# Kernel optimization log

Hardware: AMD Instinct MI355X
Metric: run time of the kernel (lower is better)

Reference implementation:

```python
import jax, jax.numpy as jnp
import numpy as np

B, G, FI, FO, H, W = 16, 8, 64, 64, 64, 64
N_ITER = 3


def setup_inputs() -> dict:
    key = jax.random.key(0)
    kx, kw, kb = jax.random.split(key, 3)
    x = jax.random.normal(kx, (B, G * FI, H, W), dtype=jnp.float32)
    # kaiming_normal_ on [fo*g, fi, 1, 1]: std = sqrt(2 / fan_in), fan_in = fi*1*1
    weight = jax.random.normal(kw, (FO * G, FI, 1, 1), dtype=jnp.float32) * np.sqrt(2.0 / FI)
    bias = jax.random.normal(kb, (1, FO, 1, 1), dtype=jnp.float32) * 0.01
    return {"x": x, "weight": weight, "bias": bias}


def reference(x, weight, bias):
    g, n_iter = G, N_ITER
    gfo, fi = weight.shape[:2]
    fo = gfo // g
    b, c, h, w = x.shape
    # grouped 1x1 conv == per-group channel matmul
    xg = x.reshape(b, g, fi, h, w)
    wg = weight.reshape(g, fo, fi)
    con = jnp.einsum('bgihw,gfi->bgfhw', xg, wg)  # [B, g, fo, H, W]
    beta = jnp.zeros((), dtype=x.dtype)
    for i in range(n_iter):
        alpha = jax.nn.sigmoid(beta)
        v = jnp.sum(alpha * con, axis=1, keepdims=True)  # [B, 1, fo, H, W]
        if i == n_iter - 1:
            out = v[:, 0]  # [B, fo, H, W]
            return out + bias
        beta = beta + jnp.sum(v * con, axis=2, keepdims=True)  # [B, g, 1, H, W]
```

## Files before the change

### kernel.cpp

```cpp
#include <hip/hip_runtime.h>


typedef __attribute__((ext_vector_type(8))) _Float16 half8;
typedef __attribute__((ext_vector_type(4))) float f32x4;

#define NG   8
#define NFI  64
#define NFO  64
#define HW   4096

__device__ __forceinline__ float sigmoidf_fast(float v) {
    float e = __builtin_amdgcn_exp2f(-1.44269504088896f * v);
    return __builtin_amdgcn_rcpf(1.0f + e);
}

__global__ __launch_bounds__(256)
void wconv_kernel(const float* __restrict__ w, _Float16* __restrict__ wbuf) {
    int V = blockIdx.x * 256 + threadIdx.x;
    int g    = V >> 10;
    int t    = (V >> 8) & 3;
    int c    = (V >> 6) & 3;
    int lane = V & 63;
    int pl = lane & 15, q = lane >> 4;
    const float* src = w + g * (NFO * NFI) + (t * 16 + pl) * NFI + (c & 1) * 32 + q * 8;
    half8 o;
    #pragma unroll
    for (int j = 0; j < 8; ++j) {
        float f = src[j];
        _Float16 h = (_Float16)f;
        o[j] = (c >> 1) ? (_Float16)(f - (float)h) : h;
    }
    *(half8*)(wbuf + (size_t)V * 8) = o;
}

__global__ __launch_bounds__(256, 2)
void routing_kernel(const float* __restrict__ x,
                    const _Float16* __restrict__ wbuf,
                    const float* __restrict__ bias,
                    float* __restrict__ out) {
    const int tid  = threadIdx.x;
    const int b    = blockIdx.x >> 6;
    const int p0   = (blockIdx.x & 63) << 6;
    const int lane = tid & 63;
    const int wv   = tid >> 6;
    const int pl   = lane & 15;
    const int q    = lane >> 4;
    const int pw   = wv * 16 + pl;

    __shared__ float    xlds[2][64 * 64];
    __shared__ _Float16 wlds[2][16 * 512];

    const float* xbase = x + (size_t)b * (NG * NFI) * HW;

#define MKXS(c) \
    const int   ch##c = wv * 16 + (c) * 4 + q; \
    const float* xs##c = xbase + (size_t)ch##c * HW + p0 + ((pl * 4 - 8 * (ch##c >> 3)) & 63);
    MKXS(0) MKXS(1) MKXS(2) MKXS(3)
#undef MKXS

    const int rb0 = q * 512 + ((pw + 8 * q) & 63);
    const int rb1 = 2048 + q * 512 + ((pw + 8 * q + 32) & 63);

    f32x4 acc[NG][4];
    #pragma unroll
    for (int g = 0; g < NG; ++g)
        #pragma unroll
        for (int t = 0; t < 4; ++t)
            acc[g][t] = (f32x4){0.f, 0.f, 0.f, 0.f};

#define CB   asm volatile("" ::: "memory")
#define BAR  __builtin_amdgcn_s_barrier()
#define SB0  __builtin_amdgcn_sched_barrier(0)
#define WAITV(N) asm volatile("s_waitcnt vmcnt(" #N ")" ::: "memory")

#define WSTAGE(G, BUF)                                                        \
    {                                                                         \
        const _Float16* ws_ = wbuf + (size_t)(G) * 8192 + (wv * 4) * 512 + lane * 8; \
        _Float16* wd_ = &wlds[BUF][0] + (wv * 4) * 512;                       \
        __builtin_amdgcn_global_load_lds(                                     \
            (const __attribute__((address_space(1))) void*)(ws_),             \
            (__attribute__((address_space(3))) void*)(wd_), 16, 0, 0);        \
        __builtin_amdgcn_global_load_lds(                                     \
            (const __attribute__((address_space(1))) void*)(ws_ + 512),       \
            (__attribute__((address_space(3))) void*)(wd_ + 512), 16, 0, 0);  \
        __builtin_amdgcn_global_load_lds(                                     \
            (const __attribute__((address_space(1))) void*)(ws_ + 1024),      \
            (__attribute__((address_space(3))) void*)(wd_ + 1024), 16, 0, 0); \
        __builtin_amdgcn_global_load_lds(                                     \
            (const __attribute__((address_space(1))) void*)(ws_ + 1536),      \
            (__attribute__((address_space(3))) void*)(wd_ + 1536), 16, 0, 0); \
    }

#define XSTAGE(G, BUF)                                                        \
    {                                                                         \
        const size_t go_ = (size_t)(G) * 64 * HW;                             \
        float* xd_ = &xlds[BUF][0] + (wv * 16) * 64;                          \
        __builtin_amdgcn_global_load_lds(                                     \
            (const __attribute__((address_space(1))) void*)(xs0 + go_),       \
            (__attribute__((address_space(3))) void*)(xd_), 16, 0, 0);        \
        __builtin_amdgcn_global_load_lds(                                     \
            (const __attribute__((address_space(1))) void*)(xs1 + go_),       \
            (__attribute__((address_space(3))) void*)(xd_ + 256), 16, 0, 0);  \
        __builtin_amdgcn_global_load_lds(                                     \
            (const __attribute__((address_space(1))) void*)(xs2 + go_),       \
            (__attribute__((address_space(3))) void*)(xd_ + 512), 16, 0, 0);  \
        __builtin_amdgcn_global_load_lds(                                     \
            (const __attribute__((address_space(1))) void*)(xs3 + go_),       \
            (__attribute__((address_space(3))) void*)(xd_ + 768), 16, 0, 0);  \
    }

#define XGRP(G, BUF)                                                         \
    {                                                                        \
        const float* xr0_ = &xlds[BUF][0] + rb0;                             \
        const float* xr1_ = &xlds[BUF][0] + rb1;                             \
        half8 b0, b1;                                                        \
        b0[0] = (_Float16)xr0_[0 * 64]; b0[1] = (_Float16)xr0_[1 * 64];      \
        b0[2] = (_Float16)xr0_[2 * 64]; b0[3] = (_Float16)xr0_[3 * 64];      \
        b0[4] = (_Float16)xr0_[4 * 64]; b0[5] = (_Float16)xr0_[5 * 64];      \
        b0[6] = (_Float16)xr0_[6 * 64]; b0[7] = (_Float16)xr0_[7 * 64];      \
        b1[0] = (_Float16)xr1_[0 * 64]; b1[1] = (_Float16)xr1_[1 * 64];      \
        b1[2] = (_Float16)xr1_[2 * 64]; b1[3] = (_Float16)xr1_[3 * 64];      \
        b1[4] = (_Float16)xr1_[4 * 64]; b1[5] = (_Float16)xr1_[5 * 64];      \
        b1[6] = (_Float16)xr1_[6 * 64]; b1[7] = (_Float16)xr1_[7 * 64];      \
        const _Float16* wg_ = &wlds[BUF][0] + lane * 8;                      \
        _Pragma("unroll")                                                    \
        for (int t = 0; t < 4; ++t) {                                        \
            const _Float16* wp_ = wg_ + (size_t)t * 2048;                    \
            half8 a0h = *(const half8*)(wp_);                                \
            half8 a1h = *(const half8*)(wp_ + 512);                          \
            half8 a0l = *(const half8*)(wp_ + 1024);                         \
            half8 a1l = *(const half8*)(wp_ + 1536);                         \
            acc[G][t] = __builtin_amdgcn_mfma_f32_16x16x32_f16(a0h, b0, acc[G][t], 0, 0, 0); \
            acc[G][t] = __builtin_amdgcn_mfma_f32_16x16x32_f16(a1h, b1, acc[G][t], 0, 0, 0); \
            acc[G][t] = __builtin_amdgcn_mfma_f32_16x16x32_f16(a0l, b0, acc[G][t], 0, 0, 0); \
            acc[G][t] = __builtin_amdgcn_mfma_f32_16x16x32_f16(a1l, b1, acc[G][t], 0, 0, 0); \
        }                                                                    \
    }

    WSTAGE(0, 0); XSTAGE(0, 0); CB;
    WSTAGE(1, 1); XSTAGE(1, 1); CB;

    WAITV(8); BAR; SB0; XGRP(0, 0); BAR; WSTAGE(2, 0); XSTAGE(2, 0); CB;
    WAITV(8); BAR; SB0; XGRP(1, 1); BAR; WSTAGE(3, 1); XSTAGE(3, 1); CB;
    WAITV(8); BAR; SB0; XGRP(2, 0); BAR; WSTAGE(4, 0); XSTAGE(4, 0); CB;
    WAITV(8); BAR; SB0; XGRP(3, 1); BAR; WSTAGE(5, 1); XSTAGE(5, 1); CB;
    WAITV(8); BAR; SB0; XGRP(4, 0); BAR; WSTAGE(6, 0); XSTAGE(6, 0); CB;
    WAITV(8); BAR; SB0; XGRP(5, 1); BAR; WSTAGE(7, 1); XSTAGE(7, 1); CB;
    WAITV(8); BAR; SB0; XGRP(6, 0); BAR;
    WAITV(0); BAR; SB0; XGRP(7, 1);

#undef XGRP
#undef XSTAGE
#undef WSTAGE
#undef CB
#undef BAR
#undef SB0
#undef WAITV

    float v0[4][4];
    #pragma unroll
    for (int t = 0; t < 4; ++t)
        #pragma unroll
        for (int r = 0; r < 4; ++r) {
            float s = 0.f;
            #pragma unroll
            for (int g = 0; g < NG; ++g) s += acc[g][t][r];
            v0[t][r] = 0.5f * s;
        }

    float beta[NG], alpha[NG];
    #pragma unroll
    for (int g = 0; g < NG; ++g) {
        float s = 0.f;
        #pragma unroll
        for (int t = 0; t < 4; ++t)
            #pragma unroll
            for (int r = 0; r < 4; ++r)
                s += v0[t][r] * acc[g][t][r];
        s += __shfl_xor(s, 16);
        s += __shfl_xor(s, 32);
        beta[g]  = s;
        alpha[g] = sigmoidf_fast(s);
    }

    #pragma unroll
    for (int t = 0; t < 4; ++t)
        #pragma unroll
        for (int r = 0; r < 4; ++r) {
            float s = 0.f;
            #pragma unroll
            for (int g = 0; g < NG; ++g) s += alpha[g] * acc[g][t][r];
            v0[t][r] = s;
        }
    #pragma unroll
    for (int g = 0; g < NG; ++g) {
        float s = 0.f;
        #pragma unroll
        for (int t = 0; t < 4; ++t)
            #pragma unroll
            for (int r = 0; r < 4; ++r)
                s += v0[t][r] * acc[g][t][r];
        s += __shfl_xor(s, 16);
        s += __shfl_xor(s, 32);
        beta[g] += s;
        alpha[g] = sigmoidf_fast(beta[g]);
    }

    #pragma unroll
    for (int t = 0; t < 4; ++t)
        #pragma unroll
        for (int r = 0; r < 4; ++r) {
            int f = t * 16 + q * 4 + r;
            float s = bias[f];
            #pragma unroll
            for (int g = 0; g < NG; ++g) s += alpha[g] * acc[g][t][r];
            out[((size_t)(b * NFO + f)) * HW + p0 + pw] = s;
        }
}

extern "C" void kernel_launch(void* const* d_in, const int* in_sizes, int n_in,
                              void* d_out, int out_size, void* d_ws, size_t ws_size,
                              hipStream_t stream) {
    const float* x    = (const float*)d_in[0];
    const float* w    = (const float*)d_in[1];
    const float* bias = (const float*)d_in[2];
    float* out = (float*)d_out;
    _Float16* wbuf = (_Float16*)d_ws;

    wconv_kernel<<<32, 256, 0, stream>>>(w, wbuf);
    routing_kernel<<<1024, 256, 0, stream>>>(x, wbuf, bias, out);
}
```

Before: 201.4 us.

## Fuse weight fp16 hi/lo split into routing kernel, drop separate conversion launch

Removes the standalone weight-conversion kernel and its workspace buffer. Each block now loads fp32 weights into registers, splits them into fp16 hi/lo halves in-kernel and writes them to LDS inside the existing double-buffered pipeline. This saves one kernel launch and the dependency between the two kernels. In exchange every block repeats the conversion and holds more registers, and the conversion work plus the extra LDS-write wait now sit on the per-group critical path.

```diff
diff --git a/kernel.cpp b/kernel.cpp
--- a/kernel.cpp
+++ b/kernel.cpp
@@ -14,28 +14,9 @@
     return __builtin_amdgcn_rcpf(1.0f + e);
 }
 
-__global__ __launch_bounds__(256)
-void wconv_kernel(const float* __restrict__ w, _Float16* __restrict__ wbuf) {
-    int V = blockIdx.x * 256 + threadIdx.x;
-    int g    = V >> 10;
-    int t    = (V >> 8) & 3;
-    int c    = (V >> 6) & 3;
-    int lane = V & 63;
-    int pl = lane & 15, q = lane >> 4;
-    const float* src = w + g * (NFO * NFI) + (t * 16 + pl) * NFI + (c & 1) * 32 + q * 8;
-    half8 o;
-    #pragma unroll
-    for (int j = 0; j < 8; ++j) {
-        float f = src[j];
-        _Float16 h = (_Float16)f;
-        o[j] = (c >> 1) ? (_Float16)(f - (float)h) : h;
-    }
-    *(half8*)(wbuf + (size_t)V * 8) = o;
-}
-
 __global__ __launch_bounds__(256, 2)
 void routing_kernel(const float* __restrict__ x,
-                    const _Float16* __restrict__ wbuf,
+                    const float* __restrict__ w,
                     const float* __restrict__ bias,
                     float* __restrict__ out) {
     const int tid  = threadIdx.x;
@@ -52,6 +33,8 @@
 
     const float* xbase = x + (size_t)b * (NG * NFI) * HW;
 
+    const float* wsrc = w + (size_t)(wv * 16 + pl) * NFI + q * 8;
+
 #define MKXS(c) \
     const int   ch##c = wv * 16 + (c) * 4 + q; \
     const float* xs##c = xbase + (size_t)ch##c * HW + p0 + ((pl * 4 - 8 * (ch##c >> 3)) & 63);
@@ -68,27 +51,38 @@
         for (int t = 0; t < 4; ++t)
             acc[g][t] = (f32x4){0.f, 0.f, 0.f, 0.f};
 
-#define CB   asm volatile("" ::: "memory")
-#define BAR  __builtin_amdgcn_s_barrier()
-#define SB0  __builtin_amdgcn_sched_barrier(0)
+#define CB    asm volatile("" ::: "memory")
+#define BAR   __builtin_amdgcn_s_barrier()
+#define SB0   __builtin_amdgcn_sched_barrier(0)
 #define WAITV(N) asm volatile("s_waitcnt vmcnt(" #N ")" ::: "memory")
-
-#define WSTAGE(G, BUF)                                                        \
+#define LGKM0 asm volatile("s_waitcnt lgkmcnt(0)" ::: "memory")
+
+#define WLOAD(G, NM)                                                          \
+    NM##a = *(const f32x4*)(wsrc + (size_t)(G) * 4096);                       \
+    NM##b = *(const f32x4*)(wsrc + (size_t)(G) * 4096 + 4);                   \
+    NM##c = *(const f32x4*)(wsrc + (size_t)(G) * 4096 + 32);                  \
+    NM##d = *(const f32x4*)(wsrc + (size_t)(G) * 4096 + 36);
+
+#define WCONV(G, NM)                                                          \
     {                                                                         \
-        const _Float16* ws_ = wbuf + (size_t)(G) * 8192 + (wv * 4) * 512 + lane * 8; \
-        _Float16* wd_ = &wlds[BUF][0] + (wv * 4) * 512;                       \
-        __builtin_amdgcn_global_load_lds(                                     \
-            (const __attribute__((address_space(1))) void*)(ws_),             \
-            (__attribute__((address_space(3))) void*)(wd_), 16, 0, 0);        \
-        __builtin_amdgcn_global_load_lds(                                     \
-            (const __attribute__((address_space(1))) void*)(ws_ + 512),       \
-            (__attribute__((address_space(3))) void*)(wd_ + 512), 16, 0, 0);  \
-        __builtin_amdgcn_global_load_lds(                                     \
-            (const __attribute__((address_space(1))) void*)(ws_ + 1024),      \
-            (__attribute__((address_space(3))) void*)(wd_ + 1024), 16, 0, 0); \
-        __builtin_amdgcn_global_load_lds(                                     \
-            (const __attribute__((address_space(1))) void*)(ws_ + 1536),      \
-            (__attribute__((address_space(3))) void*)(wd_ + 1536), 16, 0, 0); \
+        half8 h0_, h1_, l0_, l1_;                                             \
+        _Pragma("unroll")                                                     \
+        for (int j = 0; j < 4; ++j) {                                         \
+            float f0 = NM##a[j], f1 = NM##b[j], f2 = NM##c[j], f3 = NM##d[j]; \
+            _Float16 e0 = (_Float16)f0, e1 = (_Float16)f1;                    \
+            _Float16 e2 = (_Float16)f2, e3 = (_Float16)f3;                    \
+            h0_[j] = e0; h0_[j + 4] = e1;                                     \
+            h1_[j] = e2; h1_[j + 4] = e3;                                     \
+            l0_[j]     = (_Float16)(f0 - (float)e0);                          \
+            l0_[j + 4] = (_Float16)(f1 - (float)e1);                          \
+            l1_[j]     = (_Float16)(f2 - (float)e2);                          \
+            l1_[j + 4] = (_Float16)(f3 - (float)e3);                          \
+        }                                                                     \
+        _Float16* wd_ = &wlds[(G) & 1][0] + (wv * 4) * 512 + lane * 8;        \
+        *(half8*)(wd_)        = h0_;                                          \
+        *(half8*)(wd_ + 512)  = h1_;                                          \
+        *(half8*)(wd_ + 1024) = l0_;                                          \
+        *(half8*)(wd_ + 1536) = l1_;                                          \
     }
 
 #define XSTAGE(G, BUF)                                                        \
@@ -137,25 +131,31 @@
         }                                                                    \
     }
 
-    WSTAGE(0, 0); XSTAGE(0, 0); CB;
-    WSTAGE(1, 1); XSTAGE(1, 1); CB;
-
-    WAITV(8); BAR; SB0; XGRP(0, 0); BAR; WSTAGE(2, 0); XSTAGE(2, 0); CB;
-    WAITV(8); BAR; SB0; XGRP(1, 1); BAR; WSTAGE(3, 1); XSTAGE(3, 1); CB;
-    WAITV(8); BAR; SB0; XGRP(2, 0); BAR; WSTAGE(4, 0); XSTAGE(4, 0); CB;
-    WAITV(8); BAR; SB0; XGRP(3, 1); BAR; WSTAGE(5, 1); XSTAGE(5, 1); CB;
-    WAITV(8); BAR; SB0; XGRP(4, 0); BAR; WSTAGE(6, 0); XSTAGE(6, 0); CB;
-    WAITV(8); BAR; SB0; XGRP(5, 1); BAR; WSTAGE(7, 1); XSTAGE(7, 1); CB;
-    WAITV(8); BAR; SB0; XGRP(6, 0); BAR;
-    WAITV(0); BAR; SB0; XGRP(7, 1);
+    f32x4 Waa, Wab, Wac, Wad;
+    f32x4 Wba, Wbb, Wbc, Wbd;
+#define Wa_a Waa
+
+    WLOAD(0, Wa) CB; XSTAGE(0, 0); CB;
+    WLOAD(1, Wb) CB; XSTAGE(1, 1); CB;
+
+    WAITV(8); WCONV(0, Wa) LGKM0; BAR; SB0; XGRP(0, 0); BAR; WLOAD(2, Wa) CB; XSTAGE(2, 0); CB;
+    WAITV(8); WCONV(1, Wb) LGKM0; BAR; SB0; XGRP(1, 1); BAR; WLOAD(3, Wb) CB; XSTAGE(3, 1); CB;
+    WAITV(8); WCONV(2, Wa) LGKM0; BAR; SB0; XGRP(2, 0); BAR; WLOAD(4, Wa) CB; XSTAGE(4, 0); CB;
+    WAITV(8); WCONV(3, Wb) LGKM0; BAR; SB0; XGRP(3, 1); BAR; WLOAD(5, Wb) CB; XSTAGE(5, 1); CB;
+    WAITV(8); WCONV(4, Wa) LGKM0; BAR; SB0; XGRP(4, 0); BAR; WLOAD(6, Wa) CB; XSTAGE(6, 0); CB;
+    WAITV(8); WCONV(5, Wb) LGKM0; BAR; SB0; XGRP(5, 1); BAR; WLOAD(7, Wb) CB; XSTAGE(7, 1); CB;
+    WAITV(8); WCONV(6, Wa) LGKM0; BAR; SB0; XGRP(6, 0); BAR;
+    WAITV(0); WCONV(7, Wb) LGKM0; BAR; SB0; XGRP(7, 1);
 
 #undef XGRP
 #undef XSTAGE
-#undef WSTAGE
+#undef WCONV
+#undef WLOAD
 #undef CB
 #undef BAR
 #undef SB0
 #undef WAITV
+#undef LGKM0
 
     float v0[4][4];
     #pragma unroll
@@ -225,8 +225,7 @@
     const float* w    = (const float*)d_in[1];
     const float* bias = (const float*)d_in[2];
     float* out = (float*)d_out;
-    _Float16* wbuf = (_Float16*)d_ws;
-
-    wconv_kernel<<<32, 256, 0, stream>>>(w, wbuf);
-    routing_kernel<<<1024, 256, 0, stream>>>(x, wbuf, bias, out);
+    (void)d_ws; (void)ws_size;
+
+    routing_kernel<<<1024, 256, 0, stream>>>(x, w, bias, out);
 }
```

Measured after the change: 201.2 us. No clear change (-0.1%).
